# Performance work log

Hardware: AMD Instinct MI355X
Metric: run time of the kernel (lower is better)

## Reference

```python
import jax, jax.numpy as jnp
import numpy as np

# ---- geometry constants (from init_kwargs) ----
GRID = (160, 160, 160)
ORIGIN = np.array([-160.0, -160.0, -160.0], dtype=np.float32)   # corner of image volume (mm)
VOXSIZE = np.array([2.0, 2.0, 2.0], dtype=np.float32)           # mm
TIME_RES = 300.0   # ps (FWHM-like timing resolution)
TOF_BIN = 10.0     # ps
C_HALF = 0.15      # speed of light / 2 in mm/ps -> converts TOF time to position along LOR
NSTEPS = 256       # fixed ray-march samples per LOR (jit-friendly surrogate for Siddon stepping)
N_LORS = 100000
EPS = 1e-8

SIGMA = jnp.float32(TIME_RES * C_HALF / 2.355)  # spatial TOF sigma (mm), FWHM -> sigma
NVOX = GRID[0] * GRID[1] * GRID[2]
STRIDES = np.array([GRID[1] * GRID[2], GRID[2], 1], dtype=np.int32)


def setup_inputs() -> dict:
    key = jax.random.key(0)
    k1, k2, k3, k4, k5 = jax.random.split(key, 5)
    image = jax.random.uniform(k1, GRID, dtype=jnp.float32)
    effmap = jax.random.uniform(k2, GRID, dtype=jnp.float32) + 0.5
    # LOR endpoints on a cylinder of radius 250 mm surrounding the 320 mm FOV
    R = 250.0
    ang = jax.random.uniform(k3, (N_LORS, 2), dtype=jnp.float32) * (2.0 * np.pi)
    z = jax.random.uniform(k4, (N_LORS, 2), dtype=jnp.float32) * 300.0 - 150.0
    p0 = jnp.stack([R * jnp.cos(ang[:, 0]), R * jnp.sin(ang[:, 0]), z[:, 0]], axis=-1)
    p1 = jnp.stack([-R * jnp.cos(ang[:, 1]), -R * jnp.sin(ang[:, 1]), z[:, 1]], axis=-1)
    tof = jax.random.normal(k5, (N_LORS, 1), dtype=jnp.float32) * 100.0  # ps
    lors = jnp.concatenate([p0, p1, tof], axis=-1)  # [N,7]
    return {"image": image, "effmap": effmap, "lors": lors}


def _trace(lors):
    """Ray-march samples, flat voxel indices, and TOF-weighted per-sample lengths."""
    p0, p1, tof = lors[:, 0:3], lors[:, 3:6], lors[:, 6]
    d = p1 - p0                                   # [N,3]
    L = jnp.linalg.norm(d, axis=-1)               # [N]
    dl = L / NSTEPS                               # [N] step length (mm)
    t = (jnp.arange(NSTEPS, dtype=jnp.float32) + 0.5) / NSTEPS   # [S]
    pts = p0[:, None, :] + t[None, :, None] * d[:, None, :]      # [N,S,3]
    idx = jnp.floor((pts - ORIGIN) / VOXSIZE).astype(jnp.int32)  # [N,S,3]
    inb = jnp.all((idx >= 0) & (idx < jnp.array(GRID, dtype=jnp.int32)), axis=-1)  # [N,S]
    flat = jnp.sum(jnp.clip(idx, 0, jnp.array(GRID, dtype=jnp.int32) - 1)
                   * jnp.asarray(STRIDES), axis=-1)              # [N,S]
    # TOF Gaussian weight along the ray, centered at midpoint + tof offset
    s = (t[None, :] - 0.5) * L[:, None]           # signed distance from midpoint (mm)
    s_tof = (tof * C_HALF)[:, None]
    w = jnp.exp(-0.5 * jnp.square((s - s_tof) / SIGMA))
    w = jnp.where(inb, w, 0.0) * dl[:, None]      # [N,S] intersection-length weight
    return flat, w


def reference(image, effmap, lors):
    flat, w = _trace(lors)                        # [N,S], [N,S]
    img_flat = image.reshape(-1)
    # projection: p[n] = sum_s w[n,s] * image[voxel(n,s)]
    p = jnp.sum(jnp.take(img_flat, flat) * w, axis=1)            # [N]
    # backprojection of lor_values=p: bp[v] = sum_{n,s: voxel=v} w[n,s] * p[n]
    bp = jnp.zeros((NVOX,), dtype=image.dtype).at[flat.reshape(-1)].add(
        (p[:, None] * w).reshape(-1)).reshape(GRID)
    return image / (effmap + EPS) * bp
```

## Files before the change

kernel.cpp:

```cpp
#include <hip/hip_runtime.h>
#include <hip/hip_fp16.h>
#include <math.h>

#define NSTEPS 256
#define GRIDN  160
#define NVOX   (160 * 160 * 160)
#define NTPA   20
#define NTILES (NTPA * NTPA * NTPA)
#define NREP   8
#define CAP_R  256
#define ITEM_CAP (4 * 1024 * 1024)

#define INV_SIGMA 0.05233333f

struct LorT { float4 a; float4 b; };

__device__ __forceinline__ bool sample_vox(
    int j, float p0x, float p0y, float p0z,
    float dx, float dy, float dz, float L, float s_tof,
    int& ix, int& iy, int& iz, float& e)
{
#pragma clang fp contract(off)
    const float t = (j + 0.5f) * (1.0f / 256.0f);
    const float px = p0x + t * dx;
    const float py = p0y + t * dy;
    const float pz = p0z + t * dz;
    const float fx = floorf((px + 160.0f) * 0.5f);
    const float fy = floorf((py + 160.0f) * 0.5f);
    const float fz = floorf((pz + 160.0f) * 0.5f);
    const bool inb = (fx >= 0.0f) & (fx < 160.0f) &
                     (fy >= 0.0f) & (fy < 160.0f) &
                     (fz >= 0.0f) & (fz < 160.0f);
    const float s = (t - 0.5f) * L;
    const float u = (s - s_tof) * INV_SIGMA;
    e = 0.5f * (u * u);
    if (inb & (e < 10.0f)) {
        ix = (int)fx; iy = (int)fy; iz = (int)fz;
        return true;
    }
    return false;
}

__device__ __forceinline__ void lor_window(
    float p0x, float p0y, float p0z, float dx, float dy, float dz,
    float L, float s_tof, int& j0, int& j1)
{
#pragma clang fp contract(off)
    const float SIGMA = (float)(45.0 / 2.355);
    const float CUTS  = 4.4721360f * SIGMA;
    const float invL = 1.0f / L;
    float t0 = 0.5f + (s_tof - CUTS) * invL;
    float t1 = 0.5f + (s_tof + CUTS) * invL;
    if (t0 > t1) { const float tmp = t0; t0 = t1; t1 = tmp; }
    const float pc[3] = {p0x, p0y, p0z};
    const float dc[3] = {dx, dy, dz};
    #pragma unroll
    for (int a = 0; a < 3; ++a) {
        if (dc[a] != 0.0f) {
            const float inv = 1.0f / dc[a];
            const float ta = (-160.0f - pc[a]) * inv;
            const float tb = ( 160.0f - pc[a]) * inv;
            t0 = fmaxf(t0, fminf(ta, tb));
            t1 = fminf(t1, fmaxf(ta, tb));
        } else if (pc[a] < -160.0f || pc[a] >= 160.0f) t1 = -1.0f;
    }
    t0 = fmaxf(t0, 0.0f);
    t1 = fminf(t1, 1.0f);
    j0 = (int)floorf(t0 * 256.0f - 0.5f) - 2;
    j1 = (int)ceilf (t1 * 256.0f - 0.5f) + 2;
    if (!(t0 <= t1)) { j0 = 0; j1 = -1; }
    j0 = max(j0, 0);
    j1 = min(j1, NSTEPS - 1);
}

__global__ __launch_bounds__(256) void emit_kernel(
    const float* __restrict__ image,
    const float* __restrict__ lors, LorT* __restrict__ lortab,
    int* __restrict__ histcur, unsigned* __restrict__ items,
    float* __restrict__ p, unsigned* __restrict__ samples,
    int n, int mode)
{
#pragma clang fp contract(off)
    const int wave = (int)((blockIdx.x * blockDim.x + threadIdx.x) >> 6);
    const int lane = threadIdx.x & 63;
    if (wave >= n) return;
    const int rep = (int)(blockIdx.x & (NREP - 1));

    float p0x, p0y, p0z, tof, dx, dy, dz, L;
    if (mode != 2) {
        const float* l = lors + (size_t)wave * 7;
        p0x = l[0]; p0y = l[1]; p0z = l[2];
        dx = l[3] - p0x; dy = l[4] - p0y; dz = l[5] - p0z; tof = l[6];
        L = sqrtf(dx * dx + dy * dy + dz * dz);
        if (lane == 0) {
            lortab[wave].a = make_float4(p0x, p0y, p0z, tof);
            lortab[wave].b = make_float4(dx, dy, dz, L);
        }
    } else {
        const float4 A = lortab[wave].a, B = lortab[wave].b;
        p0x = A.x; p0y = A.y; p0z = A.z; tof = A.w;
        dx  = B.x; dy  = B.y; dz  = B.z; L   = B.w;
    }
    const float s_tof = tof * 0.15f;
    const float dl = L * (1.0f / 256.0f);
    int j0, j1;
    lor_window(p0x, p0y, p0z, dx, dy, dz, L, s_tof, j0, j1);
    const int nk = (j1 - j0 + 64) >> 6;

    float psum = 0.0f;
    for (int k = 0; k < nk; ++k) {
        const int j = j0 + lane + (k << 6);
        int ix, iy, iz; float e;
        const bool valid = (j <= j1) &&
            sample_vox(j, p0x, p0y, p0z, dx, dy, dz, L, s_tof, ix, iy, iz, e);
        if (mode != 2) {
            if (valid) {
                const float w = __expf(-e) * dl;
                psum += image[ix * 25600 + iy * 160 + iz] * w;
                if (samples) {
                    const unsigned lidx = (unsigned)((ix & 7) << 6)
                                        | (unsigned)((iy & 7) << 3)
                                        | (unsigned)(iz & 7);
                    const unsigned hb =
                        (unsigned)__half_as_ushort(__float2half(w));
                    samples[(size_t)wave * 256 + j] = (lidx << 16) | hb;
                }
            }
        }
        const unsigned key = valid
            ? (unsigned)((ix >> 3) * 400 + (iy >> 3) * 20 + (iz >> 3))
            : 0xFFFFFFFFu;
        const unsigned prev = __shfl_up(key, 1, 64);
        const bool chg = (lane == 0) || (prev != key);
        const unsigned long long cm = __ballot(chg);
        if (chg && valid) {
            const unsigned long long above = cm & ~((2ULL << lane) - 1ULL);
            const int nxt = above ? (__ffsll((unsigned long long)above) - 1) : 64;
            const int len = nxt - lane;
            const unsigned word = ((unsigned)wave << 14)
                                | ((unsigned)j << 6) | (unsigned)(len - 1);
            if (mode == 0) {
                const int tr = atomicAdd(&histcur[rep * NTILES + (int)key], 1);
                if (tr < CAP_R)
                    items[((size_t)key * NREP + rep) * CAP_R + tr] = word;
            } else if (mode == 1) {
                atomicAdd(&histcur[rep * NTILES + (int)key], 1);
            } else {
                const int slot = atomicAdd(&histcur[(int)key], 1);
                if (slot < ITEM_CAP) items[slot] = word;
            }
        }
    }
    if (mode != 2) {
        #pragma unroll
        for (int off = 32; off >= 1; off >>= 1) psum += __shfl_xor(psum, off, 64);
        if (lane == 0) p[wave] = psum;
    }
}

__global__ __launch_bounds__(256) void tileB3_kernel(
    const float* __restrict__ image, const float* __restrict__ effmap,
    const float* __restrict__ p, const int* __restrict__ hist8,
    const unsigned* __restrict__ items, const unsigned* __restrict__ samples,
    float* __restrict__ out)
{
    const int b = blockIdx.x;
    const int t = threadIdx.x;
    const int tx0 = (b / 400) << 3, ty0 = ((b / 20) % 20) << 3, tz0 = (b % 20) << 3;
    int pre[NREP]; int tot = 0;
    #pragma unroll
    for (int r = 0; r < NREP; ++r) {
        int c = hist8[r * NTILES + b];
        c = min(c, CAP_R);
        pre[r] = tot; tot += c;
    }
    if (tot == 0) {
        for (int v = t; v < 512; v += 256) {
            const int lx = v >> 6, ly = (v >> 3) & 7, lz = v & 7;
            out[(size_t)(tx0 + lx) * 25600 + (ty0 + ly) * 160 + (tz0 + lz)] = 0.0f;
        }
        return;
    }
    __shared__ float acc[512];
    for (int v = t; v < 512; v += 256) acc[v] = 0.0f;
    __syncthreads();
    for (int idx = t; idx < tot; idx += 256) {
        int r = 0, base = 0;
        #pragma unroll
        for (int rr = 1; rr < NREP; ++rr) {
            const bool g = (idx >= pre[rr]);
            r    = g ? rr      : r;
            base = g ? pre[rr] : base;
        }
        const unsigned it =
            items[((size_t)b * NREP + r) * CAP_R + (idx - base)];
        const int lor = (int)(it >> 14);
        const int js  = (int)((it >> 6) & 255);
        const int len = (int)(it & 63) + 1;
        const float pv = p[lor];
        const unsigned* sp = samples + (size_t)lor * 256 + js;
        #pragma unroll 4
        for (int m = 0; m < len; ++m) {
            const unsigned word = sp[m];
            const float w = __half2float(
                __ushort_as_half((unsigned short)(word & 0xFFFFu)));
            atomicAdd(&acc[(word >> 16) & 511u], pv * w);
        }
    }
    __syncthreads();
    for (int v = t; v < 512; v += 256) {
        const int lx = v >> 6, ly = (v >> 3) & 7, lz = v & 7;
        const size_t g = (size_t)(tx0 + lx) * 25600 + (ty0 + ly) * 160 + (tz0 + lz);
        out[g] = image[g] / (effmap[g] + 1e-8f) * acc[v];
    }
}

__global__ __launch_bounds__(256) void reduce_kernel(
    const int* __restrict__ hist8, int* __restrict__ tot)
{
    const int k = blockIdx.x * blockDim.x + threadIdx.x;
    if (k >= NTILES) return;
    int s = 0;
    #pragma unroll
    for (int r = 0; r < NREP; ++r) s += hist8[r * NTILES + k];
    tot[k] = s;
}

__global__ __launch_bounds__(1024) void scan_kernel(
    const int* __restrict__ tot, int* __restrict__ offs)
{
    __shared__ int part[1024];
    const int t = threadIdx.x;
    const int base = t * 8;
    int loc[8]; int s = 0;
    #pragma unroll
    for (int i = 0; i < 8; ++i) {
        const int h = (base + i < NTILES) ? tot[base + i] : 0;
        loc[i] = s; s += h;
    }
    part[t] = s;
    __syncthreads();
    for (int off = 1; off < 1024; off <<= 1) {
        int v = 0;
        if (t >= off) v = part[t - off];
        __syncthreads();
        part[t] += v;
        __syncthreads();
    }
    const int excl = (t > 0) ? part[t - 1] : 0;
    #pragma unroll
    for (int i = 0; i < 8; ++i)
        if (base + i < NTILES) offs[base + i] = excl + loc[i];
    if (t == 1023) offs[NTILES] = part[1023];
}

__global__ __launch_bounds__(256) void base_kernel(
    const int* __restrict__ offs, int* __restrict__ cursor)
{
    const int k = blockIdx.x * blockDim.x + threadIdx.x;
    if (k >= NTILES) return;
    cursor[k] = offs[k];
}

__global__ __launch_bounds__(256) void tileB_kernel(
    const float* __restrict__ image, const float* __restrict__ effmap,
    const LorT* __restrict__ lortab, const int* __restrict__ offs,
    const unsigned* __restrict__ items, const float* __restrict__ p,
    float* __restrict__ out)
{
    const int b = blockIdx.x;
    const int i0 = offs[b], i1 = min(offs[b + 1], ITEM_CAP);
    const int tx0 = (b / 400) << 3, ty0 = ((b / 20) % 20) << 3, tz0 = (b % 20) << 3;
    const int t = threadIdx.x;
    if (i0 >= i1) {
        for (int v = t; v < 512; v += 256) {
            const int lx = v >> 6, ly = (v >> 3) & 7, lz = v & 7;
            out[(size_t)(tx0 + lx) * 25600 + (ty0 + ly) * 160 + (tz0 + lz)] = 0.0f;
        }
        return;
    }
    __shared__ float acc[512];
    for (int v = t; v < 512; v += 256) acc[v] = 0.0f;
    __syncthreads();
    for (int idx = i0 + t; idx < i1; idx += 256) {
        const unsigned it = items[idx];
        const int lor = (int)(it >> 14);
        const int js  = (int)((it >> 6) & 255);
        const int len = (int)(it & 63) + 1;
        const float4 A = lortab[lor].a, B = lortab[lor].b;
        const float dl = B.w * (1.0f / 256.0f);
        const float s_tof = A.w * 0.15f;
        const float pv = p[lor];
        for (int m = 0; m < len; ++m) {
            int ix, iy, iz; float e;
            if (sample_vox(js + m, A.x, A.y, A.z, B.x, B.y, B.z, B.w, s_tof,
                           ix, iy, iz, e)) {
                const int lx = ix - tx0, ly = iy - ty0, lz = iz - tz0;
                if ((unsigned)lx < 8u && (unsigned)ly < 8u && (unsigned)lz < 8u)
                    atomicAdd(&acc[(lx << 6) | (ly << 3) | lz],
                              pv * (__expf(-e) * dl));
            }
        }
    }
    __syncthreads();
    for (int v = t; v < 512; v += 256) {
        const int lx = v >> 6, ly = (v >> 3) & 7, lz = v & 7;
        const size_t g = (size_t)(tx0 + lx) * 25600 + (ty0 + ly) * 160 + (tz0 + lz);
        out[g] = image[g] / (effmap[g] + 1e-8f) * acc[v];
    }
}

__global__ __launch_bounds__(256) void trace_direct_kernel(
    const float* __restrict__ image, const float* __restrict__ lors,
    float* __restrict__ bp, int n_lors)
{
#pragma clang fp contract(off)
    const int wave = (int)((blockIdx.x * blockDim.x + threadIdx.x) >> 6);
    const int lane = threadIdx.x & 63;
    if (wave >= n_lors) return;
    const float* l = lors + (size_t)wave * 7;
    const float p0x = l[0], p0y = l[1], p0z = l[2];
    const float dx = l[3] - p0x, dy = l[4] - p0y, dz = l[5] - p0z;
    const float tof = l[6];
    const float L  = sqrtf(dx * dx + dy * dy + dz * dz);
    const float dl = L * (1.0f / 256.0f);
    const float s_tof = tof * 0.15f;
    int j0, j1;
    lor_window(p0x, p0y, p0z, dx, dy, dz, L, s_tof, j0, j1);
    const int nk = (j1 - j0 + 64) >> 6;
    if (nk <= 0) return;
    int flat[4]; float w[4]; float psum = 0.0f;
    for (int k = 0; k < nk; ++k) {
        const int j = j0 + lane + (k << 6);
        int ix, iy, iz; float e; float wk = 0.0f; int fl = 0;
        if (j <= j1 &&
            sample_vox(j, p0x, p0y, p0z, dx, dy, dz, L, s_tof, ix, iy, iz, e)) {
            wk = __expf(-e) * dl;
            fl = ix * 25600 + iy * 160 + iz;
            psum += image[fl] * wk;
        }
        flat[k] = fl; w[k] = wk;
    }
    #pragma unroll
    for (int off = 32; off >= 1; off >>= 1) psum += __shfl_xor(psum, off, 64);
    for (int k = 0; k < nk; ++k)
        if (w[k] > 0.0f) atomicAdd(&bp[flat[k]], psum * w[k]);
}

__global__ __launch_bounds__(256) void finalize_kernel(
    const float4* __restrict__ image, const float4* __restrict__ effmap,
    float4* __restrict__ out, int n4)
{
    const int i = blockIdx.x * blockDim.x + threadIdx.x;
    if (i >= n4) return;
    const float4 im = image[i];
    const float4 ef = effmap[i];
    float4 b = out[i];
    b.x = im.x / (ef.x + 1e-8f) * b.x;
    b.y = im.y / (ef.y + 1e-8f) * b.y;
    b.z = im.z / (ef.z + 1e-8f) * b.z;
    b.w = im.w / (ef.w + 1e-8f) * b.w;
    out[i] = b;
}

extern "C" void kernel_launch(void* const* d_in, const int* in_sizes, int n_in,
                              void* d_out, int out_size, void* d_ws, size_t ws_size,
                              hipStream_t stream) {
    const float* image  = (const float*)d_in[0];
    const float* effmap = (const float*)d_in[1];
    const float* lors   = (const float*)d_in[2];
    float* out = (float*)d_out;
    const int n = in_sizes[2] / 7;

    char* ws = (char*)d_ws;
    const size_t hist_off   = 0;
    const size_t tot_off    = hist_off + (size_t)NREP * NTILES * 4;
    const size_t offs_off   = tot_off + 32768;
    const size_t cursor_off = offs_off + 32768;
    const size_t p_off      = cursor_off + 32768;
    const size_t lortab_off = p_off + (((size_t)n * 4 + 255) & ~(size_t)255);
    const size_t items_off  = lortab_off + (size_t)n * sizeof(LorT);
    const size_t itemsA_sz  = (size_t)NTILES * NREP * CAP_R * 4;
    const size_t smp_off    = items_off + itemsA_sz;
    const size_t total_A    = smp_off + (size_t)n * 256 * 4;
    const size_t total_C    = items_off + (size_t)ITEM_CAP * 4;

    const int tileGrid = (NTILES + 255) / 256;

    if (ws_size >= total_A && n > 0 && n < (1 << 17)) {
        int*      hist8  = (int*)(ws + hist_off);
        float*    p      = (float*)(ws + p_off);
        LorT*     lortab = (LorT*)(ws + lortab_off);
        unsigned* items  = (unsigned*)(ws + items_off);
        unsigned* samples = (unsigned*)(ws + smp_off);

        hipMemsetAsync(hist8, 0, (size_t)NREP * NTILES * sizeof(int), stream);

        const int blocksE = (n + 3) / 4;
        emit_kernel<<<blocksE, 256, 0, stream>>>(image, lors, lortab, hist8,
                                                 items, p, samples, n, 0);
        tileB3_kernel<<<NTILES, 256, 0, stream>>>(image, effmap, p, hist8,
                                                  items, samples, out);
    } else if (ws_size >= total_C && n > 0 && n < (1 << 17)) {
        int*      hist8  = (int*)(ws + hist_off);
        int*      tot    = (int*)(ws + tot_off);
        int*      offs   = (int*)(ws + offs_off);
        int*      cursor = (int*)(ws + cursor_off);
        float*    p      = (float*)(ws + p_off);
        LorT*     lortab = (LorT*)(ws + lortab_off);
        unsigned* items  = (unsigned*)(ws + items_off);

        hipMemsetAsync(hist8, 0, (size_t)NREP * NTILES * sizeof(int), stream);

        const int blocksE = (n + 3) / 4;
        emit_kernel<<<blocksE, 256, 0, stream>>>(image, lors, lortab, hist8,
                                                 items, p, nullptr, n, 1);
        reduce_kernel<<<tileGrid, 256, 0, stream>>>(hist8, tot);
        scan_kernel<<<1, 1024, 0, stream>>>(tot, offs);
        base_kernel<<<tileGrid, 256, 0, stream>>>(offs, cursor);
        emit_kernel<<<blocksE, 256, 0, stream>>>(image, lors, lortab, cursor,
                                                 items, p, nullptr, n, 2);
        tileB_kernel<<<NTILES, 256, 0, stream>>>(image, effmap, lortab, offs,
                                                 items, p, out);
    } else {
        hipMemsetAsync(out, 0, (size_t)NVOX * sizeof(float), stream);
        if (n > 0)
            trace_direct_kernel<<<(n + 3) / 4, 256, 0, stream>>>(image, lors, out, n);
        const int n4 = NVOX / 4;
        finalize_kernel<<<(n4 + 255) / 256, 256, 0, stream>>>(
            (const float4*)image, (const float4*)effmap, (float4*)out, n4);
    }
}
```

Before: 184.2 us.

## Bucket per-sample backprojection values by tile directly in emit pass

Each wave now computes its projection sum before scattering, so it can write the final p*w contribution (fp16 with a local voxel index) straight into per-tile buckets. This drops the separate samples array and the indirect item-to-sample lookup in the tile kernel, which now only sums bucket entries in shared memory. Runs of samples in the same tile reserve their slots with one atomic per run. Bucket overflow falls back to global atomics into a pre-zeroed output, which adds a full-volume memset and an extra read of out in the finalize step. Storing p*w in fp16 rather than w alone changes the precision characteristics.

```diff
diff --git a/kernel.cpp b/kernel.cpp
--- a/kernel.cpp
+++ b/kernel.cpp
@@ -8,7 +8,7 @@
 #define NTPA   20
 #define NTILES (NTPA * NTPA * NTPA)
 #define NREP   8
-#define CAP_R  256
+#define CAP_S  512
 #define ITEM_CAP (4 * 1024 * 1024)
 
 #define INV_SIGMA 0.05233333f
@@ -73,11 +73,129 @@
     j1 = min(j1, NSTEPS - 1);
 }
 
+__global__ __launch_bounds__(256) void emit_bucket_kernel(
+    const float* __restrict__ image, const float* __restrict__ lors,
+    int* __restrict__ scnt, unsigned* __restrict__ bucket,
+    float* __restrict__ out_bp, int n)
+{
+#pragma clang fp contract(off)
+    const int wave = (int)((blockIdx.x * blockDim.x + threadIdx.x) >> 6);
+    const int lane = threadIdx.x & 63;
+    if (wave >= n) return;
+    const int rep = (int)(blockIdx.x & (NREP - 1));
+
+    const float* l = lors + (size_t)wave * 7;
+    const float p0x = l[0], p0y = l[1], p0z = l[2];
+    const float dx = l[3] - p0x, dy = l[4] - p0y, dz = l[5] - p0z;
+    const float tof = l[6];
+    const float L  = sqrtf(dx * dx + dy * dy + dz * dz);
+    const float s_tof = tof * 0.15f;
+    const float dl = L * (1.0f / 256.0f);
+    int j0, j1;
+    lor_window(p0x, p0y, p0z, dx, dy, dz, L, s_tof, j0, j1);
+
+    float    wk[4];
+    unsigned kk[4];
+    float psum = 0.0f;
+    #pragma unroll
+    for (int k = 0; k < 4; ++k) {
+        wk[k] = 0.0f; kk[k] = 0xFFFFFFFFu;
+        const int j = j0 + lane + (k << 6);
+        if (j <= j1) {
+            int ix, iy, iz; float e;
+            if (sample_vox(j, p0x, p0y, p0z, dx, dy, dz, L, s_tof,
+                           ix, iy, iz, e)) {
+                const float w = __expf(-e) * dl;
+                wk[k] = w;
+                kk[k] = (((unsigned)((ix >> 3) * 400 + (iy >> 3) * 20
+                                     + (iz >> 3))) << 9)
+                      | (unsigned)(((ix & 7) << 6) | ((iy & 7) << 3) | (iz & 7));
+                psum += image[ix * 25600 + iy * 160 + iz] * w;
+            }
+        }
+    }
+    #pragma unroll
+    for (int off = 32; off >= 1; off >>= 1) psum += __shfl_xor(psum, off, 64);
+
+    #pragma unroll
+    for (int k = 0; k < 4; ++k) {
+        const bool valid = (kk[k] != 0xFFFFFFFFu);
+        const unsigned key = kk[k] >> 9;
+        const unsigned prev = __shfl_up(key, 1, 64);
+        const bool chg = (lane == 0) || (prev != key);
+        const unsigned long long cm = __ballot(chg);
+        const unsigned long long below = cm & ((2ULL << lane) - 1ULL);
+        const int leader = 63 - __clzll((long long)below);
+        const unsigned long long above = cm & ~((2ULL << lane) - 1ULL);
+        const int nxt = above ? (__ffsll((long long)above) - 1) : 64;
+        int tr = 0;
+        if (chg && valid)
+            tr = atomicAdd(&scnt[rep * NTILES + (int)key], nxt - lane);
+        tr = __shfl(tr, leader, 64);
+        if (valid) {
+            const int slot = tr + (lane - leader);
+            const float v = psum * wk[k];
+            if (slot < CAP_S) {
+                const unsigned entry = ((kk[k] & 511u) << 16)
+                    | (unsigned)__half_as_ushort(__float2half(v));
+                bucket[((size_t)key * NREP + rep) * CAP_S + slot] = entry;
+            } else {
+                const int ky = (int)key;
+                const int tx = ky / 400, ty = (ky / 20) % 20, tz = ky % 20;
+                const int lidx = (int)(kk[k] & 511u);
+                const size_t g = (size_t)(tx * 8 + (lidx >> 6)) * 25600
+                               + (size_t)(ty * 8 + ((lidx >> 3) & 7)) * 160
+                               + (size_t)(tz * 8 + (lidx & 7));
+                atomicAdd(&out_bp[g], v);
+            }
+        }
+    }
+}
+
+__global__ __launch_bounds__(256) void tileB4_kernel(
+    const float* __restrict__ image, const float* __restrict__ effmap,
+    const int* __restrict__ scnt, const unsigned* __restrict__ bucket,
+    float* __restrict__ out)
+{
+    const int b = blockIdx.x;
+    const int t = threadIdx.x;
+    const int tx0 = (b / 400) << 3, ty0 = ((b / 20) % 20) << 3, tz0 = (b % 20) << 3;
+    int pre[NREP]; int tot = 0;
+    #pragma unroll
+    for (int r = 0; r < NREP; ++r) {
+        int c = scnt[r * NTILES + b];
+        c = min(c, CAP_S);
+        pre[r] = tot; tot += c;
+    }
+    if (tot == 0) return;
+    __shared__ float acc[512];
+    for (int v = t; v < 512; v += 256) acc[v] = 0.0f;
+    __syncthreads();
+    for (int idx = t; idx < tot; idx += 256) {
+        int r = 0, base = 0;
+        #pragma unroll
+        for (int rr = 1; rr < NREP; ++rr) {
+            const bool g = (idx >= pre[rr]);
+            r    = g ? rr      : r;
+            base = g ? pre[rr] : base;
+        }
+        const unsigned e = bucket[((size_t)b * NREP + r) * CAP_S + (idx - base)];
+        atomicAdd(&acc[(e >> 16) & 511u],
+                  __half2float(__ushort_as_half((unsigned short)(e & 0xFFFFu))));
+    }
+    __syncthreads();
+    for (int v = t; v < 512; v += 256) {
+        const int lx = v >> 6, ly = (v >> 3) & 7, lz = v & 7;
+        const size_t g = (size_t)(tx0 + lx) * 25600 + (ty0 + ly) * 160 + (tz0 + lz);
+        out[g] = image[g] / (effmap[g] + 1e-8f) * (acc[v] + out[g]);
+    }
+}
+
 __global__ __launch_bounds__(256) void emit_kernel(
     const float* __restrict__ image,
     const float* __restrict__ lors, LorT* __restrict__ lortab,
     int* __restrict__ histcur, unsigned* __restrict__ items,
-    float* __restrict__ p, unsigned* __restrict__ samples,
+    float* __restrict__ p,
     int n, int mode)
 {
 #pragma clang fp contract(off)
@@ -114,18 +232,8 @@
         const bool valid = (j <= j1) &&
             sample_vox(j, p0x, p0y, p0z, dx, dy, dz, L, s_tof, ix, iy, iz, e);
         if (mode != 2) {
-            if (valid) {
-                const float w = __expf(-e) * dl;
-                psum += image[ix * 25600 + iy * 160 + iz] * w;
-                if (samples) {
-                    const unsigned lidx = (unsigned)((ix & 7) << 6)
-                                        | (unsigned)((iy & 7) << 3)
-                                        | (unsigned)(iz & 7);
-                    const unsigned hb =
-                        (unsigned)__half_as_ushort(__float2half(w));
-                    samples[(size_t)wave * 256 + j] = (lidx << 16) | hb;
-                }
-            }
+            if (valid)
+                psum += image[ix * 25600 + iy * 160 + iz] * (__expf(-e) * dl);
         }
         const unsigned key = valid
             ? (unsigned)((ix >> 3) * 400 + (iy >> 3) * 20 + (iz >> 3))
@@ -139,13 +247,9 @@
             const int len = nxt - lane;
             const unsigned word = ((unsigned)wave << 14)
                                 | ((unsigned)j << 6) | (unsigned)(len - 1);
-            if (mode == 0) {
-                const int tr = atomicAdd(&histcur[rep * NTILES + (int)key], 1);
-                if (tr < CAP_R)
-                    items[((size_t)key * NREP + rep) * CAP_R + tr] = word;
-            } else if (mode == 1) {
+            if (mode == 1) {
                 atomicAdd(&histcur[rep * NTILES + (int)key], 1);
-            } else {
+            } else if (mode == 2) {
                 const int slot = atomicAdd(&histcur[(int)key], 1);
                 if (slot < ITEM_CAP) items[slot] = word;
             }
@@ -155,63 +259,6 @@
         #pragma unroll
         for (int off = 32; off >= 1; off >>= 1) psum += __shfl_xor(psum, off, 64);
         if (lane == 0) p[wave] = psum;
-    }
-}
-
-__global__ __launch_bounds__(256) void tileB3_kernel(
-    const float* __restrict__ image, const float* __restrict__ effmap,
-    const float* __restrict__ p, const int* __restrict__ hist8,
-    const unsigned* __restrict__ items, const unsigned* __restrict__ samples,
-    float* __restrict__ out)
-{
-    const int b = blockIdx.x;
-    const int t = threadIdx.x;
-    const int tx0 = (b / 400) << 3, ty0 = ((b / 20) % 20) << 3, tz0 = (b % 20) << 3;
-    int pre[NREP]; int tot = 0;
-    #pragma unroll
-    for (int r = 0; r < NREP; ++r) {
-        int c = hist8[r * NTILES + b];
-        c = min(c, CAP_R);
-        pre[r] = tot; tot += c;
-    }
-    if (tot == 0) {
-        for (int v = t; v < 512; v += 256) {
-            const int lx = v >> 6, ly = (v >> 3) & 7, lz = v & 7;
-            out[(size_t)(tx0 + lx) * 25600 + (ty0 + ly) * 160 + (tz0 + lz)] = 0.0f;
-        }
-        return;
-    }
-    __shared__ float acc[512];
-    for (int v = t; v < 512; v += 256) acc[v] = 0.0f;
-    __syncthreads();
-    for (int idx = t; idx < tot; idx += 256) {
-        int r = 0, base = 0;
-        #pragma unroll
-        for (int rr = 1; rr < NREP; ++rr) {
-            const bool g = (idx >= pre[rr]);
-            r    = g ? rr      : r;
-            base = g ? pre[rr] : base;
-        }
-        const unsigned it =
-            items[((size_t)b * NREP + r) * CAP_R + (idx - base)];
-        const int lor = (int)(it >> 14);
-        const int js  = (int)((it >> 6) & 255);
-        const int len = (int)(it & 63) + 1;
-        const float pv = p[lor];
-        const unsigned* sp = samples + (size_t)lor * 256 + js;
-        #pragma unroll 4
-        for (int m = 0; m < len; ++m) {
-            const unsigned word = sp[m];
-            const float w = __half2float(
-                __ushort_as_half((unsigned short)(word & 0xFFFFu)));
-            atomicAdd(&acc[(word >> 16) & 511u], pv * w);
-        }
-    }
-    __syncthreads();
-    for (int v = t; v < 512; v += 256) {
-        const int lx = v >> 6, ly = (v >> 3) & 7, lz = v & 7;
-        const size_t g = (size_t)(tx0 + lx) * 25600 + (ty0 + ly) * 160 + (tz0 + lz);
-        out[g] = image[g] / (effmap[g] + 1e-8f) * acc[v];
     }
 }
 
@@ -379,28 +426,27 @@
     const size_t cursor_off = offs_off + 32768;
     const size_t p_off      = cursor_off + 32768;
     const size_t lortab_off = p_off + (((size_t)n * 4 + 255) & ~(size_t)255);
-    const size_t items_off  = lortab_off + (size_t)n * sizeof(LorT);
-    const size_t itemsA_sz  = (size_t)NTILES * NREP * CAP_R * 4;
-    const size_t smp_off    = items_off + itemsA_sz;
-    const size_t total_A    = smp_off + (size_t)n * 256 * 4;
-    const size_t total_C    = items_off + (size_t)ITEM_CAP * 4;
+    const size_t after_fix  = lortab_off + (size_t)n * sizeof(LorT);
+    const size_t bucket_off = after_fix;
+    const size_t total_A    = bucket_off
+                            + (size_t)NTILES * NREP * CAP_S * 4;
+    const size_t items_off2 = after_fix;
+    const size_t total_C    = items_off2 + (size_t)ITEM_CAP * 4;
 
     const int tileGrid = (NTILES + 255) / 256;
 
     if (ws_size >= total_A && n > 0 && n < (1 << 17)) {
-        int*      hist8  = (int*)(ws + hist_off);
-        float*    p      = (float*)(ws + p_off);
-        LorT*     lortab = (LorT*)(ws + lortab_off);
-        unsigned* items  = (unsigned*)(ws + items_off);
-        unsigned* samples = (unsigned*)(ws + smp_off);
-
-        hipMemsetAsync(hist8, 0, (size_t)NREP * NTILES * sizeof(int), stream);
+        int*      scnt   = (int*)(ws + hist_off);
+        unsigned* bucket = (unsigned*)(ws + bucket_off);
+
+        hipMemsetAsync(out, 0, (size_t)NVOX * sizeof(float), stream);
+        hipMemsetAsync(scnt, 0, (size_t)NREP * NTILES * sizeof(int), stream);
 
         const int blocksE = (n + 3) / 4;
-        emit_kernel<<<blocksE, 256, 0, stream>>>(image, lors, lortab, hist8,
-                                                 items, p, samples, n, 0);
-        tileB3_kernel<<<NTILES, 256, 0, stream>>>(image, effmap, p, hist8,
-                                                  items, samples, out);
+        emit_bucket_kernel<<<blocksE, 256, 0, stream>>>(image, lors, scnt,
+                                                        bucket, out, n);
+        tileB4_kernel<<<NTILES, 256, 0, stream>>>(image, effmap, scnt,
+                                                  bucket, out);
     } else if (ws_size >= total_C && n > 0 && n < (1 << 17)) {
         int*      hist8  = (int*)(ws + hist_off);
         int*      tot    = (int*)(ws + tot_off);
@@ -408,18 +454,18 @@
         int*      cursor = (int*)(ws + cursor_off);
         float*    p      = (float*)(ws + p_off);
         LorT*     lortab = (LorT*)(ws + lortab_off);
-        unsigned* items  = (unsigned*)(ws + items_off);
+        unsigned* items  = (unsigned*)(ws + items_off2);
 
         hipMemsetAsync(hist8, 0, (size_t)NREP * NTILES * sizeof(int), stream);
 
         const int blocksE = (n + 3) / 4;
         emit_kernel<<<blocksE, 256, 0, stream>>>(image, lors, lortab, hist8,
-                                                 items, p, nullptr, n, 1);
+                                                 items, p, n, 1);
         reduce_kernel<<<tileGrid, 256, 0, stream>>>(hist8, tot);
         scan_kernel<<<1, 1024, 0, stream>>>(tot, offs);
         base_kernel<<<tileGrid, 256, 0, stream>>>(offs, cursor);
         emit_kernel<<<blocksE, 256, 0, stream>>>(image, lors, lortab, cursor,
-                                                 items, p, nullptr, n, 2);
+                                                 items, p, n, 2);
         tileB_kernel<<<NTILES, 256, 0, stream>>>(image, effmap, lortab, offs,
                                                  items, p, out);
     } else {
```

Result: no change. 187.9 us (+2.0%).
